# Kernel optimization log

Measured on AMD Instinct MI355X. Metric: run time of the kernel, lower is better.

Reference implementation:

```python
import jax, jax.numpy as jnp
import numpy as np

N = 50000
E = 800000
F_IN = 128
HID = 64
HEADS = 4
NUM_TYPES = 1
NEG_SLOPE = 0.2


def setup_inputs() -> dict:
    key = jax.random.key(0)
    ks = jax.random.split(key, 20)
    s = 0.05
    inp = {
        "node_features": jax.random.normal(ks[0], (N, F_IN), jnp.float32),
        "node_types": jax.random.randint(ks[1], (N,), 0, NUM_TYPES, jnp.int32),
        "edge_index": jax.random.randint(ks[2], (2, E), 0, N, jnp.int32),
        # params
        "type_emb": jax.random.normal(ks[3], (NUM_TYPES, HID), jnp.float32) * s,
        "proj_w": jax.random.normal(ks[4], (F_IN, HID), jnp.float32) * s,
        "proj_b": jnp.zeros((HID,), jnp.float32),
        # GAT layer 0: in=64 -> heads*64, concat=True
        "lin_w0": jax.random.normal(ks[5], (HID, HEADS * HID), jnp.float32) * s,
        "att_src0": jax.random.normal(ks[6], (HEADS, HID), jnp.float32) * s,
        "att_dst0": jax.random.normal(ks[7], (HEADS, HID), jnp.float32) * s,
        "bias0": jnp.zeros((HEADS * HID,), jnp.float32),
        "ln_g0": jnp.ones((HEADS * HID,), jnp.float32),
        "ln_b0": jnp.zeros((HEADS * HID,), jnp.float32),
        # GAT layer 1: in=256 -> heads*64, concat=False (mean over heads)
        "lin_w1": jax.random.normal(ks[8], (HEADS * HID, HEADS * HID), jnp.float32) * s,
        "att_src1": jax.random.normal(ks[9], (HEADS, HID), jnp.float32) * s,
        "att_dst1": jax.random.normal(ks[10], (HEADS, HID), jnp.float32) * s,
        "bias1": jnp.zeros((HID,), jnp.float32),
        "ln_g1": jnp.ones((HID,), jnp.float32),
        "ln_b1": jnp.zeros((HID,), jnp.float32),
    }
    return inp


def _layer_norm(x, g, b, eps=1e-5):
    mu = jnp.mean(x, axis=-1, keepdims=True)
    var = jnp.mean(jnp.square(x - mu), axis=-1, keepdims=True)
    return (x - mu) * jax.lax.rsqrt(var + eps) * g + b


def _gat_conv(x, src, dst, lin_w, att_src, att_dst, bias, concat):
    # PyG GATConv: linear -> per-edge additive attention -> segment softmax over
    # incoming edges -> weighted scatter-sum. Self-loops already in src/dst.
    n = x.shape[0]
    H, C = att_src.shape
    h = (x @ lin_w).reshape(n, H, C)            # [N,H,C]
    a_s = jnp.sum(h * att_src[None], axis=-1)   # [N,H]
    a_d = jnp.sum(h * att_dst[None], axis=-1)   # [N,H]
    a = jax.nn.leaky_relu(a_s[src] + a_d[dst], NEG_SLOPE)  # [E,H]
    m = jax.ops.segment_max(a, dst, num_segments=n)
    e = jnp.exp(a - m[dst])
    z = jax.ops.segment_sum(e, dst, num_segments=n)
    alpha = e / z[dst]                           # [E,H]
    msg = h[src] * alpha[..., None]              # [E,H,C]
    out = jax.ops.segment_sum(msg, dst, num_segments=n)  # [N,H,C]
    if concat:
        out = out.reshape(n, H * C)
    else:
        out = out.mean(axis=1)
    return out + bias


def reference(node_features, node_types, edge_index,
              type_emb, proj_w, proj_b,
              lin_w0, att_src0, att_dst0, bias0, ln_g0, ln_b0,
              lin_w1, att_src1, att_dst1, bias1, ln_g1, ln_b1):
    n = node_features.shape[0]
    # add self loops (PyG GATConv default add_self_loops=True)
    loop = jnp.arange(n, dtype=edge_index.dtype)
    src = jnp.concatenate([edge_index[0], loop])
    dst = jnp.concatenate([edge_index[1], loop])

    x = node_features @ proj_w + proj_b + type_emb[node_types]  # [N,64]

    # layer 0: no residual (i == 0)
    x = _gat_conv(x, src, dst, lin_w0, att_src0, att_dst0, bias0, concat=True)
    x = jax.nn.relu(_layer_norm(x, ln_g0, ln_b0))  # [N,256]; dropout = identity (eval)

    # layer 1: residual shape [N,256] != output [N,64] -> residual skipped
    x = _gat_conv(x, src, dst, lin_w1, att_src1, att_dst1, bias1, concat=False)
    x = jax.nn.relu(_layer_norm(x, ln_g1, ln_b1))  # [N,64]
    return x
```

## Files before the change

### kernel.cpp

```cpp
#include <hip/hip_runtime.h>


#define BLK 256
#define FB  768

typedef __bf16 bf16x8 __attribute__((ext_vector_type(8)));
typedef __bf16 bf16x4 __attribute__((ext_vector_type(4)));
typedef float  f32x4  __attribute__((ext_vector_type(4)));


__device__ __forceinline__ void pack_body(const float* __restrict__ w,
                                          __bf16* __restrict__ wp,
                                          int K, int NC, int idx) {
  const int tot = (K >> 3) * NC;
  if (idx >= tot) return;
  int g = idx / NC, c = idx - g * NC;
#pragma unroll
  for (int j = 0; j < 8; ++j)
    wp[(size_t)idx * 8 + j] = (__bf16)w[(g * 8 + j) * NC + c];
}


__global__ __launch_bounds__(BLK) void k_prep(
    const float* __restrict__ pw, const float* __restrict__ w0,
    const float* __restrict__ w1, __bf16* __restrict__ pwp,
    __bf16* __restrict__ w0p, __bf16* __restrict__ w1p,
    int* __restrict__ cnt, int* __restrict__ sidx, int n, int nchunks) {
  int b = blockIdx.x;
  const int t = threadIdx.x;
  if (b < nchunks) {
    int i = b * BLK + t;
    if (i < n) { cnt[i] = 1; sidx[(size_t)i << 6] = i; }
    return;
  }
  b -= nchunks;
  if (b < 4)  { pack_body(pw, pwp, 128, 64,  b * BLK + t); return; }
  b -= 4;
  if (b < 8)  { pack_body(w0, w0p, 64, 256,  b * BLK + t); return; }
  b -= 8;
  pack_body(w1, w1p, 256, 256, b * BLK + t);
}


__global__ __launch_bounds__(BLK) void k_fill_projlin0(
    const int* __restrict__ src, const int* __restrict__ dst,
    int* __restrict__ cnt, int* __restrict__ sidx, int E,
    const float* __restrict__ nf, const int* __restrict__ types,
    const __bf16* __restrict__ pwp, const float* __restrict__ pb,
    const float* __restrict__ emb,
    const __bf16* __restrict__ w0p,
    const float* __restrict__ asrc0, const float* __restrict__ adst0,
    __bf16* __restrict__ H, float* __restrict__ as_, float* __restrict__ ad_,
    int n) {
  __shared__ __bf16 xt[64][72];
  if (blockIdx.x < FB) {
    const int st = FB * BLK;
    for (int e = blockIdx.x * BLK + threadIdx.x; e < E; e += 4 * st) {
      const int e1 = e + st, e2 = e + 2 * st, e3 = e + 3 * st;
      const bool vB = e1 < E, vC = e2 < E, vD = e3 < E;
      int sA = src[e], dA = dst[e];
      int sB = 0, dB = 0, sC = 0, dC = 0, sD = 0, dD = 0;
      if (vB) { sB = src[e1]; dB = dst[e1]; }
      if (vC) { sC = src[e2]; dC = dst[e2]; }
      if (vD) { sD = src[e3]; dD = dst[e3]; }
      int slA = atomicAdd(&cnt[dA], 1);
      int slB = vB ? atomicAdd(&cnt[dB], 1) : 64;
      int slC = vC ? atomicAdd(&cnt[dC], 1) : 64;
      int slD = vD ? atomicAdd(&cnt[dD], 1) : 64;
      if (slA < 64) sidx[((size_t)dA << 6) + slA] = sA;
      if (slB < 64) sidx[((size_t)dB << 6) + slB] = sB;
      if (slC < 64) sidx[((size_t)dC << 6) + slC] = sC;
      if (slD < 64) sidx[((size_t)dD << 6) + slD] = sD;
    }
    return;
  }
  const int bid = blockIdx.x - FB;
  const int t = threadIdx.x, w = t >> 6, l = t & 63;
  const int l15 = l & 15, lg = l >> 4;
  const int m0 = bid * 64;

  {
    const int mbase = m0 + w * 16;
    f32x4 acc[4] = {};
    const int ar = mbase + l15;
    const bool av = ar < n;
#pragma unroll
    for (int ks = 0; ks < 4; ++ks) {
      bf16x8 a = {};
      if (av) {
        const float* ap = nf + (size_t)ar * 128 + ks * 32 + lg * 8;
        float4 f0 = *(const float4*)(ap);
        float4 f1 = *(const float4*)(ap + 4);
        a[0] = (__bf16)f0.x; a[1] = (__bf16)f0.y; a[2] = (__bf16)f0.z; a[3] = (__bf16)f0.w;
        a[4] = (__bf16)f1.x; a[5] = (__bf16)f1.y; a[6] = (__bf16)f1.z; a[7] = (__bf16)f1.w;
      }
#pragma unroll
      for (int nt = 0; nt < 4; ++nt) {
        int c = nt * 16 + l15;
        int g = ks * 4 + lg;
        bf16x8 b = *(const bf16x8*)(pwp + ((size_t)g * 64 + c) * 8);
        acc[nt] = __builtin_amdgcn_mfma_f32_16x16x32_bf16(a, b, acc[nt], 0, 0, 0);
      }
    }
#pragma unroll
    for (int reg = 0; reg < 4; ++reg) {
      int row = mbase + lg * 4 + reg;
      int lrow = w * 16 + lg * 4 + reg;
      if (row < n) {
        int ty = types[row];
#pragma unroll
        for (int nt = 0; nt < 4; ++nt) {
          int c = nt * 16 + l15;
          xt[lrow][c] = (__bf16)(acc[nt][reg] + pb[c] + emb[ty * 64 + c]);
        }
      } else {
#pragma unroll
        for (int nt = 0; nt < 4; ++nt) xt[lrow][nt * 16 + l15] = (__bf16)0.f;
      }
    }
  }
  __syncthreads();

  float asv[4], adv[4];
#pragma unroll
  for (int nt = 0; nt < 4; ++nt) {
    int c = w * 64 + nt * 16 + l15;
    asv[nt] = asrc0[c];
    adv[nt] = adst0[c];
  }
  f32x4 acc[4][4] = {};
  for (int ks = 0; ks < 2; ++ks) {
    bf16x8 a[4];
#pragma unroll
    for (int mt = 0; mt < 4; ++mt)
      a[mt] = *(const bf16x8*)&xt[mt * 16 + l15][ks * 32 + lg * 8];
    bf16x8 b[4];
#pragma unroll
    for (int nt = 0; nt < 4; ++nt) {
      int c = w * 64 + nt * 16 + l15;
      int g = ks * 4 + lg;
      b[nt] = *(const bf16x8*)(w0p + ((size_t)g * 256 + c) * 8);
    }
#pragma unroll
    for (int nt = 0; nt < 4; ++nt)
#pragma unroll
      for (int mt = 0; mt < 4; ++mt)
        acc[mt][nt] = __builtin_amdgcn_mfma_f32_16x16x32_bf16(a[mt], b[nt], acc[mt][nt], 0, 0, 0);
  }
#pragma unroll
  for (int mt = 0; mt < 4; ++mt) {
#pragma unroll
    for (int reg = 0; reg < 4; ++reg) {
      int row = m0 + mt * 16 + lg * 4 + reg;
      bool vr = row < n;
      float s = 0.f, d = 0.f;
      if (vr) {
#pragma unroll
        for (int nt = 0; nt < 4; ++nt) {
          float cv = acc[mt][nt][reg];
          H[(size_t)row * 256 + w * 64 + nt * 16 + l15] = (__bf16)cv;
          s = fmaf(cv, asv[nt], s);
          d = fmaf(cv, adv[nt], d);
        }
      }
#pragma unroll
      for (int o = 8; o; o >>= 1) { s += __shfl_xor(s, o); d += __shfl_xor(d, o); }
      if (l15 == 0 && vr) { as_[row * 4 + w] = s; ad_[row * 4 + w] = d; }
    }
  }
}


__global__ __launch_bounds__(BLK) void k_agg0_lin1(
    const int* __restrict__ cntA, const int* __restrict__ sidx,
    const float* __restrict__ as0, const float* __restrict__ ad0,
    const __bf16* __restrict__ h0,
    const float* __restrict__ bias, const float* __restrict__ g,
    const float* __restrict__ b,
    const __bf16* __restrict__ w1p,
    const float* __restrict__ asrc1, const float* __restrict__ adst1,
    __bf16* __restrict__ H1, float* __restrict__ as1, float* __restrict__ ad1,
    int n) {
  __shared__ __bf16 xt[16][264];
  const int t = threadIdx.x, w = t >> 6, lane = t & 63;
  const int hsel = lane >> 4, l15 = lane & 15;
  const int gbase = blockIdx.x * 16;
  const float4 bias4 = ((const float4*)bias)[lane];
  const float4 g4 = ((const float4*)g)[lane];
  const float4 b4 = ((const float4*)b)[lane];

  for (int q = 0; q < 4; ++q) {
    const int d = gbase + w * 4 + q;
    const int lrow = w * 4 + q;
    if (d < n) {
      int cnt = cntA[d]; if (cnt > 64) cnt = 64;
      const int* sp = sidx + ((size_t)d << 6);
      const float adv = ad0[d * 4 + hsel];
      float ax = 0.f, ay = 0.f, az = 0.f, aw = 0.f, z = 0.f;
      int j = 0;
      for (; j + 4 <= cnt; j += 4) {
        int4 s4 = *(const int4*)(sp + j);
        int s0 = __builtin_amdgcn_readfirstlane(s4.x);
        int s1 = __builtin_amdgcn_readfirstlane(s4.y);
        int s2 = __builtin_amdgcn_readfirstlane(s4.z);
        int s3 = __builtin_amdgcn_readfirstlane(s4.w);
        float q0 = as0[s0 * 4 + hsel], q1 = as0[s1 * 4 + hsel];
        float q2 = as0[s2 * 4 + hsel], q3 = as0[s3 * 4 + hsel];
        bf16x4 v0 = *(const bf16x4*)(h0 + (size_t)s0 * 256 + lane * 4);
        bf16x4 v1 = *(const bf16x4*)(h0 + (size_t)s1 * 256 + lane * 4);
        bf16x4 v2 = *(const bf16x4*)(h0 + (size_t)s2 * 256 + lane * 4);
        bf16x4 v3 = *(const bf16x4*)(h0 + (size_t)s3 * 256 + lane * 4);
        float a;
        a = q0 + adv; a = fmaxf(a, 0.2f * a); float e0 = __expf(a);
        a = q1 + adv; a = fmaxf(a, 0.2f * a); float e1 = __expf(a);
        a = q2 + adv; a = fmaxf(a, 0.2f * a); float e2 = __expf(a);
        a = q3 + adv; a = fmaxf(a, 0.2f * a); float e3 = __expf(a);
        z += (e0 + e1) + (e2 + e3);
        ax = fmaf(e0, (float)v0[0], ax); ay = fmaf(e0, (float)v0[1], ay);
        az = fmaf(e0, (float)v0[2], az); aw = fmaf(e0, (float)v0[3], aw);
        ax = fmaf(e1, (float)v1[0], ax); ay = fmaf(e1, (float)v1[1], ay);
        az = fmaf(e1, (float)v1[2], az); aw = fmaf(e1, (float)v1[3], aw);
        ax = fmaf(e2, (float)v2[0], ax); ay = fmaf(e2, (float)v2[1], ay);
        az = fmaf(e2, (float)v2[2], az); aw = fmaf(e2, (float)v2[3], aw);
        ax = fmaf(e3, (float)v3[0], ax); ay = fmaf(e3, (float)v3[1], ay);
        az = fmaf(e3, (float)v3[2], az); aw = fmaf(e3, (float)v3[3], aw);
      }
      for (; j < cnt; ++j) {
        int s = __builtin_amdgcn_readfirstlane(sp[j]);
        float a = as0[s * 4 + hsel] + adv; a = fmaxf(a, 0.2f * a);
        float e = __expf(a);
        z += e;
        bf16x4 hv = *(const bf16x4*)(h0 + (size_t)s * 256 + lane * 4);
        ax = fmaf(e, (float)hv[0], ax); ay = fmaf(e, (float)hv[1], ay);
        az = fmaf(e, (float)hv[2], az); aw = fmaf(e, (float)hv[3], aw);
      }
      float rz = 1.f / z;
      float vx = ax * rz + bias4.x, vy = ay * rz + bias4.y;
      float vz = az * rz + bias4.z, vw = aw * rz + bias4.w;
      float s1 = vx + vy + vz + vw;
#pragma unroll
      for (int o = 32; o; o >>= 1) s1 += __shfl_xor(s1, o);
      float mu = s1 * (1.f / 256.f);
      float dx = vx - mu, dy = vy - mu, dz = vz - mu, dw = vw - mu;
      float qq = dx * dx + dy * dy + dz * dz + dw * dw;
#pragma unroll
      for (int o = 32; o; o >>= 1) qq += __shfl_xor(qq, o);
      float is = rsqrtf(qq * (1.f / 256.f) + 1e-5f);
      bf16x4 o4;
      o4[0] = (__bf16)fmaxf(dx * is * g4.x + b4.x, 0.f);
      o4[1] = (__bf16)fmaxf(dy * is * g4.y + b4.y, 0.f);
      o4[2] = (__bf16)fmaxf(dz * is * g4.z + b4.z, 0.f);
      o4[3] = (__bf16)fmaxf(dw * is * g4.w + b4.w, 0.f);
      *(bf16x4*)&xt[lrow][lane * 4] = o4;
    } else {
      bf16x4 zf = {};
      *(bf16x4*)&xt[lrow][lane * 4] = zf;
    }
  }
  __syncthreads();

  const int lg = hsel;
  float asv[4], adv[4];
#pragma unroll
  for (int nt = 0; nt < 4; ++nt) {
    int c = w * 64 + nt * 16 + l15;
    asv[nt] = asrc1[c];
    adv[nt] = adst1[c];
  }
  f32x4 acc[4] = {};
  for (int ks = 0; ks < 8; ++ks) {
    bf16x8 a = *(const bf16x8*)&xt[l15][ks * 32 + lg * 8];
#pragma unroll
    for (int nt = 0; nt < 4; ++nt) {
      int c = w * 64 + nt * 16 + l15;
      int g = ks * 4 + lg;
      bf16x8 bb = *(const bf16x8*)(w1p + ((size_t)g * 256 + c) * 8);
      acc[nt] = __builtin_amdgcn_mfma_f32_16x16x32_bf16(a, bb, acc[nt], 0, 0, 0);
    }
  }
#pragma unroll
  for (int reg = 0; reg < 4; ++reg) {
    int row = gbase + lg * 4 + reg;
    bool vr = row < n;
    float s = 0.f, d = 0.f;
    if (vr) {
#pragma unroll
      for (int nt = 0; nt < 4; ++nt) {
        float cv = acc[nt][reg];
        H1[(size_t)row * 256 + w * 64 + nt * 16 + l15] = (__bf16)cv;
        s = fmaf(cv, asv[nt], s);
        d = fmaf(cv, adv[nt], d);
      }
    }
#pragma unroll
    for (int o = 8; o; o >>= 1) { s += __shfl_xor(s, o); d += __shfl_xor(d, o); }
    if (l15 == 0 && vr) { as1[row * 4 + w] = s; ad1[row * 4 + w] = d; }
  }
}


__global__ __launch_bounds__(BLK) void k_agg1(
    const int* __restrict__ cntA, const int* __restrict__ sidx,
    const float* __restrict__ as_, const float* __restrict__ ad_,
    const __bf16* __restrict__ h1,
    const float* __restrict__ bias, const float* __restrict__ g,
    const float* __restrict__ b, float* __restrict__ out, int n) {
  const int lane = threadIdx.x & 63;
  const int wid = (blockIdx.x * BLK + threadIdx.x) >> 6;
  const int nw = (gridDim.x * BLK) >> 6;
  const int hsel = lane >> 4;
  const int p = lane & 15;
  const float4 bias4 = ((const float4*)bias)[p];
  const float4 g4 = ((const float4*)g)[p];
  const float4 b4 = ((const float4*)b)[p];
  for (int d = wid; d < n; d += nw) {
    int cnt = cntA[d]; if (cnt > 64) cnt = 64;
    const int* sp = sidx + ((size_t)d << 6);
    const float adv = ad_[d * 4 + hsel];
    float ax = 0.f, ay = 0.f, az = 0.f, aw = 0.f, z = 0.f;
    int j = 0;
    for (; j + 4 <= cnt; j += 4) {
      int4 s4 = *(const int4*)(sp + j);
      int s0 = __builtin_amdgcn_readfirstlane(s4.x);
      int s1 = __builtin_amdgcn_readfirstlane(s4.y);
      int s2 = __builtin_amdgcn_readfirstlane(s4.z);
      int s3 = __builtin_amdgcn_readfirstlane(s4.w);
      float q0 = as_[s0 * 4 + hsel], q1 = as_[s1 * 4 + hsel];
      float q2 = as_[s2 * 4 + hsel], q3 = as_[s3 * 4 + hsel];
      bf16x4 v0 = *(const bf16x4*)(h1 + (size_t)s0 * 256 + lane * 4);
      bf16x4 v1 = *(const bf16x4*)(h1 + (size_t)s1 * 256 + lane * 4);
      bf16x4 v2 = *(const bf16x4*)(h1 + (size_t)s2 * 256 + lane * 4);
      bf16x4 v3 = *(const bf16x4*)(h1 + (size_t)s3 * 256 + lane * 4);
      float a;
      a = q0 + adv; a = fmaxf(a, 0.2f * a); float e0 = __expf(a);
      a = q1 + adv; a = fmaxf(a, 0.2f * a); float e1 = __expf(a);
      a = q2 + adv; a = fmaxf(a, 0.2f * a); float e2 = __expf(a);
      a = q3 + adv; a = fmaxf(a, 0.2f * a); float e3 = __expf(a);
      z += (e0 + e1) + (e2 + e3);
      ax = fmaf(e0, (float)v0[0], ax); ay = fmaf(e0, (float)v0[1], ay);
      az = fmaf(e0, (float)v0[2], az); aw = fmaf(e0, (float)v0[3], aw);
      ax = fmaf(e1, (float)v1[0], ax); ay = fmaf(e1, (float)v1[1], ay);
      az = fmaf(e1, (float)v1[2], az); aw = fmaf(e1, (float)v1[3], aw);
      ax = fmaf(e2, (float)v2[0], ax); ay = fmaf(e2, (float)v2[1], ay);
      az = fmaf(e2, (float)v2[2], az); aw = fmaf(e2, (float)v2[3], aw);
      ax = fmaf(e3, (float)v3[0], ax); ay = fmaf(e3, (float)v3[1], ay);
      az = fmaf(e3, (float)v3[2], az); aw = fmaf(e3, (float)v3[3], aw);
    }
    for (; j < cnt; ++j) {
      int s = __builtin_amdgcn_readfirstlane(sp[j]);
      float a = as_[s * 4 + hsel] + adv; a = fmaxf(a, 0.2f * a);
      float e = __expf(a);
      z += e;
      bf16x4 hv = *(const bf16x4*)(h1 + (size_t)s * 256 + lane * 4);
      ax = fmaf(e, (float)hv[0], ax); ay = fmaf(e, (float)hv[1], ay);
      az = fmaf(e, (float)hv[2], az); aw = fmaf(e, (float)hv[3], aw);
    }
    float rz = 1.f / z;
    ax *= rz; ay *= rz; az *= rz; aw *= rz;
#pragma unroll
    for (int o = 16; o <= 32; o <<= 1) {
      ax += __shfl_xor(ax, o); ay += __shfl_xor(ay, o);
      az += __shfl_xor(az, o); aw += __shfl_xor(aw, o);
    }
    float vx = 0.25f * ax + bias4.x, vy = 0.25f * ay + bias4.y;
    float vz = 0.25f * az + bias4.z, vw = 0.25f * aw + bias4.w;
    float s1 = vx + vy + vz + vw;
#pragma unroll
    for (int o = 8; o; o >>= 1) s1 += __shfl_xor(s1, o);
    float mu = s1 * (1.f / 64.f);
    float dx = vx - mu, dy = vy - mu, dz = vz - mu, dw = vw - mu;
    float q = dx * dx + dy * dy + dz * dz + dw * dw;
#pragma unroll
    for (int o = 8; o; o >>= 1) q += __shfl_xor(q, o);
    float is = rsqrtf(q * (1.f / 64.f) + 1e-5f);
    if (lane < 16) {
      float4 o4;
      o4.x = fmaxf(dx * is * g4.x + b4.x, 0.f);
      o4.y = fmaxf(dy * is * g4.y + b4.y, 0.f);
      o4.z = fmaxf(dz * is * g4.z + b4.z, 0.f);
      o4.w = fmaxf(dw * is * g4.w + b4.w, 0.f);
      ((float4*)(out + (size_t)d * 64))[p] = o4;
    }
  }
}

extern "C" void kernel_launch(void* const* d_in, const int* in_sizes, int n_in,
                              void* d_out, int out_size, void* d_ws, size_t ws_size,
                              hipStream_t stream) {
  const float* nf    = (const float*)d_in[0];
  const int*   types = (const int*)d_in[1];
  const int*   ei    = (const int*)d_in[2];
  const float* emb   = (const float*)d_in[3];
  const float* pw    = (const float*)d_in[4];
  const float* pb    = (const float*)d_in[5];
  const float* w0    = (const float*)d_in[6];
  const float* asrc0 = (const float*)d_in[7];
  const float* adst0 = (const float*)d_in[8];
  const float* b0    = (const float*)d_in[9];
  const float* g0    = (const float*)d_in[10];
  const float* be0   = (const float*)d_in[11];
  const float* w1    = (const float*)d_in[12];
  const float* asrc1 = (const float*)d_in[13];
  const float* adst1 = (const float*)d_in[14];
  const float* b1    = (const float*)d_in[15];
  const float* g1    = (const float*)d_in[16];
  const float* be1   = (const float*)d_in[17];

  const int n = in_sizes[0] / 128;
  const int E = in_sizes[2] / 2;
  const int* srcI = ei;
  const int* dstI = ei + E;

  float* W = (float*)d_ws;
  size_t o = 0;
  __bf16* h0b = (__bf16*)(W + o); o += (size_t)n * 128;
  __bf16* h1b = (__bf16*)(W + o); o += (size_t)n * 128;
  float* as0 = W + o;             o += (size_t)n * 4;
  float* ad0 = W + o;             o += (size_t)n * 4;
  float* as1 = W + o;             o += (size_t)n * 4;
  float* ad1 = W + o;             o += (size_t)n * 4;
  __bf16* w0p = (__bf16*)(W + o); o += 64 * 256 / 2;
  __bf16* w1p = (__bf16*)(W + o); o += 256 * 256 / 2;
  __bf16* pwp = (__bf16*)(W + o); o += 128 * 64 / 2;
  int* I = (int*)(W + o);
  size_t io = 0;
  int* cnt  = I + io; io += n;
  int* sidx = I + io; io += (size_t)n * 64;

  const int nchunks = (n + BLK - 1) / BLK;
  const int mgrid = (n + 63) / 64;
  const int ggrid = (n + 15) / 16;
  const int agrid = (n * 64 + BLK - 1) / BLK;

  k_prep<<<nchunks + 44, BLK, 0, stream>>>(pw, w0, w1, pwp, w0p, w1p, cnt, sidx, n, nchunks);
  k_fill_projlin0<<<FB + mgrid, BLK, 0, stream>>>(srcI, dstI, cnt, sidx, E,
                                                  nf, types, pwp, pb, emb,
                                                  w0p, asrc0, adst0, h0b, as0, ad0, n);
  k_agg0_lin1<<<ggrid, BLK, 0, stream>>>(cnt, sidx, as0, ad0, h0b, b0, g0, be0,
                                         w1p, asrc1, adst1, h1b, as1, ad1, n);
  k_agg1<<<agrid, BLK, 0, stream>>>(cnt, sidx, as1, ad1, h1b, b1, g1, be1,
                                    (float*)d_out, n);
}
```

Before: 245.6 us.

## Make layer-1 linear wave-local to drop block barrier in agg0_lin1

Each wave now aggregates 8 nodes into its own shared-memory tile and then runs the full 256-column layer-1 GEMM for those rows itself, so the block-wide __syncthreads is gone. Waves no longer wait on the slowest wave's gather before starting MFMA work. The cost is that half of each 16-row MFMA tile is padding (only 8 of 16 rows are valid), which doubles the MFMA and weight-load work per node. Each wave also reads the whole w1p matrix instead of a quarter of it.

Result: slower. 255.0 us (+3.8%).

```diff
diff --git a/kernel.cpp b/kernel.cpp
--- a/kernel.cpp
+++ b/kernel.cpp
@@ -3,6 +3,7 @@
 
 #define BLK 256
 #define FB  768
+#define NPW 8
 
 typedef __bf16 bf16x8 __attribute__((ext_vector_type(8)));
 typedef __bf16 bf16x4 __attribute__((ext_vector_type(4)));
@@ -181,17 +182,17 @@
     const float* __restrict__ asrc1, const float* __restrict__ adst1,
     __bf16* __restrict__ H1, float* __restrict__ as1, float* __restrict__ ad1,
     int n) {
-  __shared__ __bf16 xt[16][264];
+  __shared__ __bf16 xt[4][NPW][264];
   const int t = threadIdx.x, w = t >> 6, lane = t & 63;
   const int hsel = lane >> 4, l15 = lane & 15;
-  const int gbase = blockIdx.x * 16;
+  const int lg = hsel;
+  const int base = (blockIdx.x * 4 + w) * NPW;
   const float4 bias4 = ((const float4*)bias)[lane];
   const float4 g4 = ((const float4*)g)[lane];
   const float4 b4 = ((const float4*)b)[lane];
 
-  for (int q = 0; q < 4; ++q) {
-    const int d = gbase + w * 4 + q;
-    const int lrow = w * 4 + q;
+  for (int q = 0; q < NPW; ++q) {
+    const int d = base + q;
     if (d < n) {
       int cnt = cntA[d]; if (cnt > 64) cnt = 64;
       const int* sp = sidx + ((size_t)d << 6);
@@ -251,50 +252,50 @@
       o4[1] = (__bf16)fmaxf(dy * is * g4.y + b4.y, 0.f);
       o4[2] = (__bf16)fmaxf(dz * is * g4.z + b4.z, 0.f);
       o4[3] = (__bf16)fmaxf(dw * is * g4.w + b4.w, 0.f);
-      *(bf16x4*)&xt[lrow][lane * 4] = o4;
+      *(bf16x4*)&xt[w][q][lane * 4] = o4;
     } else {
-      bf16x4 zf = {};
-      *(bf16x4*)&xt[lrow][lane * 4] = zf;
-    }
-  }
-  __syncthreads();
-
-  const int lg = hsel;
-  float asv[4], adv[4];
-#pragma unroll
-  for (int nt = 0; nt < 4; ++nt) {
-    int c = w * 64 + nt * 16 + l15;
-    asv[nt] = asrc1[c];
-    adv[nt] = adst1[c];
-  }
-  f32x4 acc[4] = {};
-  for (int ks = 0; ks < 8; ++ks) {
-    bf16x8 a = *(const bf16x8*)&xt[l15][ks * 32 + lg * 8];
-#pragma unroll
-    for (int nt = 0; nt < 4; ++nt) {
-      int c = w * 64 + nt * 16 + l15;
-      int g = ks * 4 + lg;
-      bf16x8 bb = *(const bf16x8*)(w1p + ((size_t)g * 256 + c) * 8);
-      acc[nt] = __builtin_amdgcn_mfma_f32_16x16x32_bf16(a, bb, acc[nt], 0, 0, 0);
-    }
-  }
-#pragma unroll
-  for (int reg = 0; reg < 4; ++reg) {
-    int row = gbase + lg * 4 + reg;
-    bool vr = row < n;
-    float s = 0.f, d = 0.f;
-    if (vr) {
-#pragma unroll
-      for (int nt = 0; nt < 4; ++nt) {
-        float cv = acc[nt][reg];
-        H1[(size_t)row * 256 + w * 64 + nt * 16 + l15] = (__bf16)cv;
-        s = fmaf(cv, asv[nt], s);
-        d = fmaf(cv, adv[nt], d);
-      }
-    }
-#pragma unroll
-    for (int o = 8; o; o >>= 1) { s += __shfl_xor(s, o); d += __shfl_xor(d, o); }
-    if (l15 == 0 && vr) { as1[row * 4 + w] = s; ad1[row * 4 + w] = d; }
+      bf16x4 zf4 = {};
+      *(bf16x4*)&xt[w][q][lane * 4] = zf4;
+    }
+  }
+
+  const bf16x8 zf = {};
+  for (int h = 0; h < 4; ++h) {
+    float sr[4] = {0.f, 0.f, 0.f, 0.f};
+    float dr[4] = {0.f, 0.f, 0.f, 0.f};
+#pragma unroll
+    for (int ntl = 0; ntl < 4; ++ntl) {
+      const int nt = h * 4 + ntl;
+      const int c = nt * 16 + l15;
+      const float asv = asrc1[c], adv = adst1[c];
+      f32x4 acc = {};
+#pragma unroll
+      for (int ks = 0; ks < 8; ++ks) {
+        bf16x8 a = (l15 < NPW) ? *(const bf16x8*)&xt[w][l15][ks * 32 + lg * 8] : zf;
+        bf16x8 bb = *(const bf16x8*)(w1p + ((size_t)(ks * 4 + lg) * 256 + c) * 8);
+        acc = __builtin_amdgcn_mfma_f32_16x16x32_bf16(a, bb, acc, 0, 0, 0);
+      }
+#pragma unroll
+      for (int reg = 0; reg < 4; ++reg) {
+        int lr = lg * 4 + reg;
+        int row = base + lr;
+        if (lr < NPW && row < n) {
+          float cv = acc[reg];
+          H1[(size_t)row * 256 + c] = (__bf16)cv;
+          sr[reg] = fmaf(cv, asv, sr[reg]);
+          dr[reg] = fmaf(cv, adv, dr[reg]);
+        }
+      }
+    }
+#pragma unroll
+    for (int reg = 0; reg < 4; ++reg) {
+      float s = sr[reg], dd = dr[reg];
+#pragma unroll
+      for (int o = 8; o; o >>= 1) { s += __shfl_xor(s, o); dd += __shfl_xor(dd, o); }
+      int lr = lg * 4 + reg;
+      int row = base + lr;
+      if (l15 == 0 && lr < NPW && row < n) { as1[row * 4 + h] = s; ad1[row * 4 + h] = dd; }
+    }
   }
 }
 
@@ -429,7 +430,8 @@
 
   const int nchunks = (n + BLK - 1) / BLK;
   const int mgrid = (n + 63) / 64;
-  const int ggrid = (n + 15) / 16;
+  const int gwaves = (n + NPW - 1) / NPW;
+  const int ggrid = (gwaves + 3) / 4;
   const int agrid = (n * 64 + BLK - 1) / BLK;
 
   k_prep<<<nchunks + 44, BLK, 0, stream>>>(pw, w0, w1, pwp, w0p, w1p, cnt, sidx, n, nchunks);
```
